# Performance work log

Hardware: AMD Instinct MI355X
Metric: run time of the kernel (lower is better)

Reference implementation:

```python
import jax, jax.numpy as jnp
import numpy as np

N_SOURCES, SEQ_LEN, BS, INPUT_DIM = 4, 512, 16, 512


def _pairwise_dist(p, g):
    # p, g: [S, L] flattened per-source signals; Euclidean cdist [S, S]
    pn = jnp.sum(p * p, axis=-1)
    gn = jnp.sum(g * g, axis=-1)
    d2 = pn[:, None] + gn[None, :] - 2.0 * (p @ g.T)
    return jnp.sqrt(jnp.maximum(d2, 0.0))


def _greedy_match(dist):
    # Sequential greedy nearest-pair assignment (same order as argsort-rank
    # based matching in the original, since ranks are monotone in distance).
    S = dist.shape[0]

    def body(i, carry):
        d, match = carry
        m = jnp.argmin(d.reshape(-1))
        r, c = m // S, m % S
        match = match.at[r].set(c)
        d = d.at[r, :].set(jnp.inf)
        d = d.at[:, c].set(jnp.inf)
        return d, match

    _, match = jax.lax.fori_loop(0, S, body, (dist, jnp.zeros((S,), jnp.int32)))
    return match


def setup_inputs() -> dict:
    key = jax.random.key(0)
    k1, k2 = jax.random.split(key)
    preds = jax.random.normal(k1, (N_SOURCES, SEQ_LEN, BS, INPUT_DIM), dtype=jnp.float32)
    gts = jax.random.normal(k2, (N_SOURCES, BS, SEQ_LEN, INPUT_DIM), dtype=jnp.float32)
    return {"preds": preds, "gts": gts}


def reference(preds, gts):
    # preds: [S, T, B, D]; gts: [S, B, T, D]
    S, T, B, D = preds.shape
    gts_t = jnp.transpose(gts, (0, 2, 1, 3))           # [S, T, B, D] (reshape() == transpose)
    pf = jnp.transpose(preds, (2, 0, 1, 3)).reshape(B, S, T * D)   # [B, S, L]
    gf = jnp.transpose(gts_t, (2, 0, 1, 3)).reshape(B, S, T * D)   # [B, S, L]
    dists = jax.vmap(_pairwise_dist)(pf, gf)           # [B, S, S]
    matches = jax.vmap(_greedy_match)(dists)           # [B, S] pred row -> gt col
    gm = jnp.take_along_axis(gf, matches[..., None], axis=1)  # [B, S, L]
    per_src = jnp.sqrt(jnp.sum((pf - gm) ** 2, axis=-1))       # [B, S] Frobenius norm
    return jnp.sum(per_src)
```

## Files before the change

kernel.cpp:

```cpp
#include <hip/hip_runtime.h>

#define S 4
#define T 512
#define B 16
#define D 512
#define L (T * D)
#define SSTRIDE (T * B * D)

#define CHUNKS 128
#define THREADS 256
#define VEC_PER_CHUNK (L / 4 / CHUNKS)
#define ITERS (VEC_PER_CHUNK / THREADS)

#define SOFF (SSTRIDE / 4)


__global__ __launch_bounds__(THREADS) void partial_kernel(
    const float* __restrict__ preds, const float* __restrict__ gts,
    float* __restrict__ ws) {
  const int b = blockIdx.x & (B - 1);
  const int chunk = blockIdx.x >> 4;
  const int tid = threadIdx.x;

  float dot[16], pn[4], gn[4];
#pragma unroll
  for (int k = 0; k < 16; k++) dot[k] = 0.f;
#pragma unroll
  for (int k = 0; k < 4; k++) { pn[k] = 0.f; gn[k] = 0.f; }

#pragma unroll
  for (int it = 0; it < ITERS; ++it) {
    const int ivec = chunk * VEC_PER_CHUNK + it * THREADS + tid;
    const int i = ivec * 4;
    const int t = i >> 9;
    const int d = i & 511;

    const float4* pp =
        reinterpret_cast<const float4*>(preds + (size_t)t * (B * D) + (size_t)b * D + d);
    const float4* gp = reinterpret_cast<const float4*>(gts + (size_t)b * L + i);

    float4 p[4], g[4];
#pragma unroll
    for (int s = 0; s < 4; s++) p[s] = pp[(size_t)s * SOFF];
#pragma unroll
    for (int s = 0; s < 4; s++) g[s] = gp[(size_t)s * SOFF];

#pragma unroll
    for (int s = 0; s < 4; s++) {
      pn[s] += p[s].x * p[s].x + p[s].y * p[s].y + p[s].z * p[s].z + p[s].w * p[s].w;
      gn[s] += g[s].x * g[s].x + g[s].y * g[s].y + g[s].z * g[s].z + g[s].w * g[s].w;
    }
#pragma unroll
    for (int sp = 0; sp < 4; sp++) {
#pragma unroll
      for (int sg = 0; sg < 4; sg++) {
        dot[sp * 4 + sg] += p[sp].x * g[sg].x + p[sp].y * g[sg].y +
                            p[sp].z * g[sg].z + p[sp].w * g[sg].w;
      }
    }
  }

  __shared__ float red[24][4];
  const int lane = tid & 63;
  const int wave = tid >> 6;
#pragma unroll
  for (int k = 0; k < 24; k++) {
    float v = (k < 16) ? dot[k] : ((k < 20) ? pn[k - 16] : gn[k - 20]);
#pragma unroll
    for (int off = 32; off > 0; off >>= 1) v += __shfl_down(v, off, 64);
    if (lane == 0) red[k][wave] = v;
  }
  __syncthreads();
  if (tid < 24) {
    float s = red[tid][0] + red[tid][1] + red[tid][2] + red[tid][3];
    atomicAdd(&ws[b * 24 + tid], s);
  }
}

__global__ __launch_bounds__(64) void finalize_kernel(const float* __restrict__ ws,
                                                      float* __restrict__ out) {
  const int tid = threadIdx.x;
  float local = 0.f;
  if (tid < B) {
    const float* w = ws + tid * 24;
    float dist[4][4], dcur[4][4];
#pragma unroll
    for (int r = 0; r < 4; r++) {
#pragma unroll
      for (int c = 0; c < 4; c++) {
        float d2 = w[16 + r] + w[20 + c] - 2.0f * w[r * 4 + c];
        float dd = sqrtf(fmaxf(d2, 0.0f));
        dist[r][c] = dd;
        dcur[r][c] = dd;
      }
    }
    int match[4] = {0, 0, 0, 0};
    for (int it = 0; it < 4; ++it) {
      float best = INFINITY;
      int bm = 0;
      for (int r = 0; r < 4; r++)
        for (int c = 0; c < 4; c++) {
          float v = dcur[r][c];
          if (v < best) { best = v; bm = r * 4 + c; }
        }
      const int r = bm >> 2, c = bm & 3;
      match[r] = c;
      for (int k = 0; k < 4; k++) { dcur[r][k] = INFINITY; dcur[k][c] = INFINITY; }
    }
#pragma unroll
    for (int r = 0; r < 4; r++) local += dist[r][match[r]];
  }
#pragma unroll
  for (int off = 32; off > 0; off >>= 1) local += __shfl_down(local, off, 64);
  if (tid == 0) out[0] = local;
}

extern "C" void kernel_launch(void* const* d_in, const int* in_sizes, int n_in,
                              void* d_out, int out_size, void* d_ws, size_t ws_size,
                              hipStream_t stream) {
  const float* preds = (const float*)d_in[0];
  const float* gts = (const float*)d_in[1];
  float* ws = (float*)d_ws;

  hipMemsetAsync(d_ws, 0, B * 24 * sizeof(float), stream);
  partial_kernel<<<dim3(B * CHUNKS), dim3(THREADS), 0, stream>>>(preds, gts, ws);
  finalize_kernel<<<dim3(1), dim3(64), 0, stream>>>(ws, (float*)d_out);
}
```

Before: 155.3 us.

## Double-buffer input tiles in LDS via async global_load_lds per wave

Replaces direct per-thread float4 global loads with asynchronous global-to-LDS DMA into a per-wave double buffer. Each wave processes its own segment, prefetching the next tile while computing on the current one. The block-wide shared-memory reduction and barrier are replaced by per-wave atomics. This aims to hide memory latency, at the cost of extra LDS traffic and more atomics, and depends on correct waitcnt encoding.

```diff
diff --git a/kernel.cpp b/kernel.cpp
--- a/kernel.cpp
+++ b/kernel.cpp
@@ -4,23 +4,40 @@
 #define T 512
 #define B 16
 #define D 512
+#define L (T * T)
+#undef L
 #define L (T * D)
 #define SSTRIDE (T * B * D)
 
-#define CHUNKS 128
-#define THREADS 256
-#define VEC_PER_CHUNK (L / 4 / CHUNKS)
-#define ITERS (VEC_PER_CHUNK / THREADS)
+#define THREADS 128
+#define BLOCKS 1024
+#define SEGS_PER_B 128
+#define SEG_FLOATS (L / SEGS_PER_B)
+#define TILE_F 256
+#define ITERS (SEG_FLOATS / TILE_F)
 
-#define SOFF (SSTRIDE / 4)
+#define WAITCNT_VM8 0x0F78
+#define WAITCNT_VM0 0x0F70
+
+__device__ __forceinline__ void dma16(const float* gp, float* lp) {
+  __builtin_amdgcn_global_load_lds(
+      (const __attribute__((address_space(1))) void*)gp,
+      (__attribute__((address_space(3))) void*)lp, 16, 0, 0);
+}
 
 
 __global__ __launch_bounds__(THREADS) void partial_kernel(
     const float* __restrict__ preds, const float* __restrict__ gts,
     float* __restrict__ ws) {
-  const int b = blockIdx.x & (B - 1);
-  const int chunk = blockIdx.x >> 4;
+  __shared__ float tile[2][2][8][TILE_F];
+
   const int tid = threadIdx.x;
+  const int lane = tid & 63;
+  const int w = tid >> 6;
+
+  const int gw = blockIdx.x * 2 + w;
+  const int b = gw >> 7;
+  const int seg = gw & (SEGS_PER_B - 1);
 
   float dot[16], pn[4], gn[4];
 #pragma unroll
@@ -28,22 +45,36 @@
 #pragma unroll
   for (int k = 0; k < 4; k++) { pn[k] = 0.f; gn[k] = 0.f; }
 
+  auto issue = [&](int it, int buf) {
+    const int fb = seg * SEG_FLOATS + it * TILE_F;
+    const int t = fb >> 9;
+    const int d = fb & 511;
+    const float* pg = preds + (size_t)t * (B * D) + (size_t)b * D + d + lane * 4;
+    const float* gg = gts + (size_t)b * L + fb + lane * 4;
+#pragma unroll
+    for (int s = 0; s < 4; s++) {
+      dma16(pg + (size_t)s * SSTRIDE, &tile[w][buf][s][0]);
+      dma16(gg + (size_t)s * SSTRIDE, &tile[w][buf][4 + s][0]);
+    }
+  };
+
+  issue(0, 0);
 #pragma unroll
   for (int it = 0; it < ITERS; ++it) {
-    const int ivec = chunk * VEC_PER_CHUNK + it * THREADS + tid;
-    const int i = ivec * 4;
-    const int t = i >> 9;
-    const int d = i & 511;
-
-    const float4* pp =
-        reinterpret_cast<const float4*>(preds + (size_t)t * (B * D) + (size_t)b * D + d);
-    const float4* gp = reinterpret_cast<const float4*>(gts + (size_t)b * L + i);
-
+    if (it + 1 < ITERS) {
+      issue(it + 1, (it + 1) & 1);
+      __builtin_amdgcn_s_waitcnt(WAITCNT_VM8);
+    } else {
+      __builtin_amdgcn_s_waitcnt(WAITCNT_VM0);
+    }
+    const int cb = it & 1;
     float4 p[4], g[4];
 #pragma unroll
-    for (int s = 0; s < 4; s++) p[s] = pp[(size_t)s * SOFF];
+    for (int s = 0; s < 4; s++)
+      p[s] = *reinterpret_cast<const float4*>(&tile[w][cb][s][lane * 4]);
 #pragma unroll
-    for (int s = 0; s < 4; s++) g[s] = gp[(size_t)s * SOFF];
+    for (int s = 0; s < 4; s++)
+      g[s] = *reinterpret_cast<const float4*>(&tile[w][cb][4 + s][lane * 4]);
 
 #pragma unroll
     for (int s = 0; s < 4; s++) {
@@ -60,21 +91,14 @@
     }
   }
 
-  __shared__ float red[24][4];
-  const int lane = tid & 63;
-  const int wave = tid >> 6;
 #pragma unroll
   for (int k = 0; k < 24; k++) {
     float v = (k < 16) ? dot[k] : ((k < 20) ? pn[k - 16] : gn[k - 20]);
 #pragma unroll
     for (int off = 32; off > 0; off >>= 1) v += __shfl_down(v, off, 64);
-    if (lane == 0) red[k][wave] = v;
+    if (lane == 0) tile[w][0][0][k] = v;
   }
-  __syncthreads();
-  if (tid < 24) {
-    float s = red[tid][0] + red[tid][1] + red[tid][2] + red[tid][3];
-    atomicAdd(&ws[b * 24 + tid], s);
-  }
+  if (lane < 24) atomicAdd(&ws[b * 24 + lane], tile[w][0][0][lane]);
 }
 
 __global__ __launch_bounds__(64) void finalize_kernel(const float* __restrict__ ws,
@@ -123,6 +147,6 @@
   float* ws = (float*)d_ws;
 
   hipMemsetAsync(d_ws, 0, B * 24 * sizeof(float), stream);
-  partial_kernel<<<dim3(B * CHUNKS), dim3(THREADS), 0, stream>>>(preds, gts, ws);
+  partial_kernel<<<dim3(BLOCKS), dim3(THREADS), 0, stream>>>(preds, gts, ws);
   finalize_kernel<<<dim3(1), dim3(64), 0, stream>>>(ws, (float*)d_out);
 }
```

New measurement: 171.6 us. +10.5%, slower.
